# Kernel optimization log

Measured on AMD Instinct MI355X. Metric: run time of the kernel, lower is better.

The kernel has to match this reference:

```python
import jax, jax.numpy as jnp
import numpy as np

B, S, D_IN, D_OUT, H = 4, 2048, 1024, 1024, 16
HD = D_OUT // H


def setup_inputs() -> dict:
    key = jax.random.key(0)
    ks = jax.random.split(key, 6)
    sc_in = 1.0 / np.sqrt(D_IN)
    sc_out = 1.0 / np.sqrt(D_OUT)
    return {
        "x": jax.random.normal(ks[0], (B, S, D_IN), dtype=jnp.float32),
        "Wq": jax.random.normal(ks[1], (D_IN, D_OUT), dtype=jnp.float32) * sc_in,
        "Wk": jax.random.normal(ks[2], (D_IN, D_OUT), dtype=jnp.float32) * sc_in,
        "Wv": jax.random.normal(ks[3], (D_IN, D_OUT), dtype=jnp.float32) * sc_in,
        "Wp": jax.random.normal(ks[4], (D_OUT, D_OUT), dtype=jnp.float32) * sc_out,
        "bp": jax.random.normal(ks[5], (D_OUT,), dtype=jnp.float32) * 0.01,
    }


def reference(x, Wq, Wk, Wv, Wp, bp):
    b, s, _ = x.shape
    # project and split heads: [b, h, s, hd]
    q = (x @ Wq).reshape(b, s, H, HD).transpose(0, 2, 1, 3)
    k = (x @ Wk).reshape(b, s, H, HD).transpose(0, 2, 1, 3)
    v = (x @ Wv).reshape(b, s, H, HD).transpose(0, 2, 1, 3)
    # materialized [b, h, s, s] scores (faithful to the naive module)
    score = jnp.einsum("bhqd,bhkd->bhqk", q, k)
    causal = jnp.tril(jnp.ones((s, s), dtype=bool))
    score = jnp.where(causal, score, -jnp.inf)
    attn = jax.nn.softmax(score / np.sqrt(HD), axis=-1)
    ctx = jnp.einsum("bhqk,bhkd->bhqd", attn, v)
    ctx = ctx.transpose(0, 2, 1, 3).reshape(b, s, D_OUT)
    return ctx @ Wp + bp
```

## Files before the change

kernel.cpp:

```cpp
#include <hip/hip_runtime.h>
#include <hip/hip_bf16.h>
#include <stdint.h>

#define BB   4
#define SS   2048
#define DIN  1024
#define DOUT 1024
#define NH   16
#define HD   64
#define MROWS (BB * SS)

typedef __bf16 bf16x8 __attribute__((ext_vector_type(8)));
typedef float  f32x4  __attribute__((ext_vector_type(4)));

__device__ __forceinline__ unsigned short f2bf(float f) {
  union { float f; uint32_t u; } v; v.f = f;
  uint32_t u = v.u;
  uint32_t r = (u + 0x7fffu + ((u >> 16) & 1u)) >> 16;
  return (unsigned short)r;
}

__device__ __forceinline__ unsigned int cvt_pk_bf16(float lo, float hi) {
  unsigned int r;
  asm("v_cvt_pk_bf16_f32 %0, %1, %2" : "=v"(r) : "v"(lo), "v"(hi));
  return r;
}

#define GLOAD_LDS16(gsrc, ldst)                                                   \
  __builtin_amdgcn_global_load_lds(                                               \
      (const __attribute__((address_space(1))) void*)(gsrc),                      \
      (__attribute__((address_space(3))) void*)(ldst), 16, 0, 0)


__global__ void cvt_x_kernel(const float* __restrict__ in,
                             unsigned short* __restrict__ out, int n4) {
  int i = blockIdx.x * blockDim.x + threadIdx.x;
  int stride = gridDim.x * blockDim.x;
  for (; i < n4; i += stride) {
    float4 f = ((const float4*)in)[i];
    ushort4 o;
    o.x = f2bf(f.x); o.y = f2bf(f.y); o.z = f2bf(f.z); o.w = f2bf(f.w);
    ((ushort4*)out)[i] = o;
  }
}

__global__ void cvt_w_t_kernel(const float* __restrict__ w0,
                               const float* __restrict__ w1,
                               const float* __restrict__ w2,
                               const float* __restrict__ w3,
                               unsigned short* __restrict__ out) {
  __shared__ float tile[32][33];
  const float* src = (blockIdx.z == 0) ? w0 : (blockIdx.z == 1) ? w1
                   : (blockIdx.z == 2) ? w2 : w3;
  unsigned short* dst = out + (size_t)blockIdx.z * (DIN * DOUT);
  int kb = blockIdx.x * 32, nb = blockIdx.y * 32;
  tile[threadIdx.y][threadIdx.x] = src[(size_t)(kb + threadIdx.y) * DOUT + nb + threadIdx.x];
  __syncthreads();
  dst[(size_t)(nb + threadIdx.y) * DIN + kb + threadIdx.x] = f2bf(tile[threadIdx.x][threadIdx.y]);
}

__device__ __forceinline__ void gemm128_core(const unsigned short* __restrict__ A,
                                             const unsigned short* __restrict__ BT,
                                             f32x4 (&acc)[4][4]) {
  extern __shared__ __align__(16) unsigned short sm[];
  const int tid = threadIdx.x, lane = tid & 63, w = tid >> 6;
  const int wm = (w >> 1) * 64, wn = (w & 1) * 64;
  const int g = lane >> 4, c = lane & 15;

#pragma unroll
  for (int mi = 0; mi < 4; mi++)
#pragma unroll
    for (int ni = 0; ni < 4; ni++)
      acc[mi][ni] = (f32x4){0.f, 0.f, 0.f, 0.f};

  const int srow = tid >> 3;
  const int gchunk = (tid & 7) ^ (srow & 7);
  const unsigned short* Ag = A + (size_t)srow * 1024 + gchunk * 8;
  const unsigned short* Bg = BT + (size_t)srow * 1024 + gchunk * 8;
  const int dst8 = tid * 8;

#define STAGE128(kt, buf) do {                                              \
    const int _k = (kt) * 64;                                               \
    _Pragma("unroll") for (int _j = 0; _j < 4; ++_j) {                      \
      GLOAD_LDS16(Ag + (size_t)_j * 32 * 1024 + _k,                         \
                  &sm[(buf) * 8192 + _j * 2048 + dst8]);                    \
      GLOAD_LDS16(Bg + (size_t)_j * 32 * 1024 + _k,                         \
                  &sm[16384 + (buf) * 8192 + _j * 2048 + dst8]);            \
    } } while (0)

  int aoff[4][2], boff[4][2];
#pragma unroll
  for (int mi = 0; mi < 4; mi++)
#pragma unroll
    for (int k2 = 0; k2 < 2; k2++)
      aoff[mi][k2] = (wm + mi * 16 + c) * 64 + (((k2 * 4 + g) ^ (c & 7)) * 8);
#pragma unroll
  for (int ni = 0; ni < 4; ni++)
#pragma unroll
    for (int k2 = 0; k2 < 2; k2++)
      boff[ni][k2] = (wn + ni * 16 + c) * 64 + (((k2 * 4 + g) ^ (c & 7)) * 8);

  STAGE128(0, 0);
  __syncthreads();

#pragma unroll 1
  for (int t = 0; t < 16; ++t) {
    const int buf = t & 1;
    if (t + 1 < 16) STAGE128(t + 1, buf ^ 1);
    const unsigned short* As_ = sm + buf * 8192;
    const unsigned short* Bs_ = sm + 16384 + buf * 8192;
#pragma unroll
    for (int k2 = 0; k2 < 2; k2++) {
      bf16x8 a[4], b[4];
#pragma unroll
      for (int mi = 0; mi < 4; mi++) a[mi] = *(const bf16x8*)&As_[aoff[mi][k2]];
#pragma unroll
      for (int ni = 0; ni < 4; ni++) b[ni] = *(const bf16x8*)&Bs_[boff[ni][k2]];
#pragma unroll
      for (int mi = 0; mi < 4; mi++)
#pragma unroll
        for (int ni = 0; ni < 4; ni++)
          acc[mi][ni] = __builtin_amdgcn_mfma_f32_16x16x32_bf16(a[mi], b[ni], acc[mi][ni], 0, 0, 0);
    }
    __syncthreads();
  }
#undef STAGE128
}

__global__ __launch_bounds__(256, 2) void gemm_qkv_kernel(
    const unsigned short* __restrict__ xb, const unsigned short* __restrict__ wt,
    unsigned short* __restrict__ qs, unsigned short* __restrict__ kbuf,
    unsigned short* __restrict__ vt) {
  const int nT = blockIdx.x, mT = blockIdx.y, z = blockIdx.z;
  f32x4 acc[4][4];
  gemm128_core(xb + (size_t)mT * 128 * 1024,
               wt + (size_t)z * (DIN * DOUT) + (size_t)nT * 128 * 1024, acc);

  const int tid = threadIdx.x, lane = tid & 63, w = tid >> 6;
  const int wm = (w >> 1) * 64, wn = (w & 1) * 64;
  const int g = lane >> 4, c = lane & 15;
  const float scale = (z == 0) ? 0.18033688011112042f : 1.0f;

  if (z < 2) {
    unsigned short* dstQK = (z == 0) ? qs : kbuf;
#pragma unroll
    for (int mi = 0; mi < 4; mi++)
#pragma unroll
      for (int ni = 0; ni < 4; ni++) {
        int n = nT * 128 + wn + ni * 16 + c;
        int h = n >> 6, hd = n & 63;
#pragma unroll
        for (int jj = 0; jj < 4; jj++) {
          int m = mT * 128 + wm + mi * 16 + g * 4 + jj;
          int b = m >> 11, ss = m & 2047;
          dstQK[(((size_t)(b * NH + h)) * SS + ss) * HD + hd] = f2bf(acc[mi][ni][jj] * scale);
        }
      }
  } else {
#pragma unroll
    for (int mi = 0; mi < 4; mi++) {
      int m0 = mT * 128 + wm + mi * 16 + g * 4;
      int b = m0 >> 11, s0 = m0 & 2047;
#pragma unroll
      for (int ni = 0; ni < 4; ni++) {
        int n = nT * 128 + wn + ni * 16 + c;
        int h = n >> 6, hd = n & 63;
        uint2 st;
        st.x = cvt_pk_bf16(acc[mi][ni][0], acc[mi][ni][1]);
        st.y = cvt_pk_bf16(acc[mi][ni][2], acc[mi][ni][3]);
        *(uint2*)&vt[(((size_t)(b * NH + h)) * HD + hd) * SS + s0] = st;
      }
    }
  }
}

__global__ __launch_bounds__(256, 2) void gemm_out_kernel(
    const unsigned short* __restrict__ ctx, const unsigned short* __restrict__ wtp,
    const float* __restrict__ bp, float* __restrict__ out) {
  const int nT = blockIdx.x, mT = blockIdx.y;
  f32x4 acc[4][4];
  gemm128_core(ctx + (size_t)mT * 128 * 1024, wtp + (size_t)nT * 128 * 1024, acc);

  const int tid = threadIdx.x, lane = tid & 63, w = tid >> 6;
  const int wm = (w >> 1) * 64, wn = (w & 1) * 64;
  const int g = lane >> 4, c = lane & 15;
#pragma unroll
  for (int mi = 0; mi < 4; mi++)
#pragma unroll
    for (int ni = 0; ni < 4; ni++) {
      int n = nT * 128 + wn + ni * 16 + c;
      float bias = bp[n];
#pragma unroll
      for (int jj = 0; jj < 4; jj++) {
        int m = mT * 128 + wm + mi * 16 + g * 4 + jj;
        out[(size_t)m * DOUT + n] = acc[mi][ni][jj] + bias;
      }
    }
}

__global__ __launch_bounds__(512) void attn_kernel(
    const unsigned short* __restrict__ qs, const unsigned short* __restrict__ kbuf,
    const unsigned short* __restrict__ vt, unsigned short* __restrict__ ctx) {
  const int pairIdx = blockIdx.x, h = blockIdx.y, b = blockIdx.z;
  const int tid = threadIdx.x, lane = tid & 63, w = tid >> 6;
  const int g = lane >> 4, c = lane & 15;
  const size_t bh = (size_t)(b * NH + h);
  const unsigned short* Q = qs + bh * SS * HD;
  const unsigned short* K = kbuf + bh * SS * HD;
  const unsigned short* V = vt + bh * HD * SS;

  __shared__ __align__(16) unsigned short Klds[2][64 * 64];
  __shared__ __align__(16) unsigned short Vlds[2][64 * 64];

  const int srow = tid >> 3, scol = tid & 7;
  const int sK_w = ((srow & 3) << 1) | ((srow >> 4) & 1);
  const int sV_w = ((srow & 3) << 1) | ((srow >> 2) & 1);
  const int kdst = srow * 64 + ((scol ^ sK_w) * 8);
  const int vdst = srow * 64 + ((scol ^ sV_w) * 8);
  const unsigned short* Kg0 = K + (size_t)srow * HD + scol * 8;
  const unsigned short* Vg0 = V + (size_t)srow * SS + scol * 8;

  int kaoff[4][2], vaoff[4][2];
#pragma unroll
  for (int ni = 0; ni < 4; ni++) {
    int r = (c >> 2) * 16 + ni * 4 + (c & 3);
    int s = ((r & 3) << 1) | ((r >> 4) & 1);
#pragma unroll
    for (int kk = 0; kk < 2; kk++)
      kaoff[ni][kk] = r * 64 + (((kk * 4 + g) ^ s) * 8);
  }
#pragma unroll
  for (int nh = 0; nh < 4; nh++) {
    int r = nh * 16 + c;
    int s = ((r & 3) << 1) | ((r >> 2) & 1);
#pragma unroll
    for (int k2 = 0; k2 < 2; k2++)
      vaoff[nh][k2] = r * 64 + (((2 * g + k2) ^ s) * 8);
  }

#pragma unroll 1
  for (int seg = 0; seg < 2; ++seg) {
    const int qtB = (seg == 0) ? (3 - pairIdx + 4) : pairIdx;
    const int q0 = qtB * 256 + w * 32;
    const int nt = 4 * qtB + 4;
    const int ntw = q0 / 64 + 1;

    bf16x8 aq[2][2];
#pragma unroll
    for (int qf = 0; qf < 2; qf++)
#pragma unroll
      for (int kk = 0; kk < 2; kk++)
        aq[qf][kk] = *(const bf16x8*)&Q[(size_t)(q0 + qf * 16 + c) * HD + kk * 32 + g * 8];

    float m_run[2] = {-3.0e38f, -3.0e38f};
    float l_run[2] = {0.f, 0.f};
    f32x4 acc[2][4];
#pragma unroll
    for (int qf = 0; qf < 2; qf++)
#pragma unroll
      for (int nh = 0; nh < 4; nh++) acc[qf][nh] = (f32x4){0.f, 0.f, 0.f, 0.f};

    {
      uint4 k0 = *(const uint4*)Kg0;
      uint4 v0 = *(const uint4*)Vg0;
      __syncthreads();
      *(uint4*)&Klds[0][kdst] = k0;
      *(uint4*)&Vlds[0][vdst] = v0;
      __syncthreads();
    }
    int cur = 0;

#pragma unroll 1
    for (int t = 0; t < nt; ++t) {
      const bool more = (t + 1 < nt);
      uint4 knx, vnx;
      if (more) {
        knx = *(const uint4*)(Kg0 + (size_t)(t + 1) * 64 * HD);
        vnx = *(const uint4*)(Vg0 + (size_t)(t + 1) * 64);
      }
      if (t < ntw) {
        const unsigned short* Kl = Klds[cur];
        const unsigned short* Vl = Vlds[cur];
        bf16x8 ka[4][2], va[4][2];
#pragma unroll
        for (int ni = 0; ni < 4; ni++)
#pragma unroll
          for (int kk = 0; kk < 2; kk++)
            ka[ni][kk] = *(const bf16x8*)&Kl[kaoff[ni][kk]];
#pragma unroll
        for (int nh = 0; nh < 4; nh++)
#pragma unroll
          for (int k2 = 0; k2 < 2; k2++)
            va[nh][k2] = *(const bf16x8*)&Vl[vaoff[nh][k2]];

        f32x4 sv[2][4];
        __builtin_amdgcn_s_setprio(1);
#pragma unroll
        for (int qf = 0; qf < 2; qf++)
#pragma unroll
          for (int ni = 0; ni < 4; ni++) {
            f32x4 z = (f32x4){0.f, 0.f, 0.f, 0.f};
            z = __builtin_amdgcn_mfma_f32_16x16x32_bf16(ka[ni][0], aq[qf][0], z, 0, 0, 0);
            sv[qf][ni] = __builtin_amdgcn_mfma_f32_16x16x32_bf16(ka[ni][1], aq[qf][1], z, 0, 0, 0);
          }
        __builtin_amdgcn_s_setprio(0);

        if (t == ntw - 1) {
#pragma unroll
          for (int qf = 0; qf < 2; qf++) {
            int q = q0 + qf * 16 + c;
#pragma unroll
            for (int ni = 0; ni < 4; ni++)
#pragma unroll
              for (int jj = 0; jj < 4; jj++) {
                int kvv = t * 64 + g * 16 + ni * 4 + jj;
                if (kvv > q) sv[qf][ni][jj] = -3.0e38f;
              }
          }
        }

#pragma unroll
        for (int qf = 0; qf < 2; qf++) {
          float mx = sv[qf][0][0];
#pragma unroll
          for (int ni = 0; ni < 4; ni++)
#pragma unroll
            for (int jj = 0; jj < 4; jj++) mx = fmaxf(mx, sv[qf][ni][jj]);
          mx = fmaxf(mx, __shfl_xor(mx, 16));
          mx = fmaxf(mx, __shfl_xor(mx, 32));
          float mnew = fmaxf(m_run[qf], mx);
          float al = exp2f(m_run[qf] - mnew);
          m_run[qf] = mnew;
          float rs = 0.f;
#pragma unroll
          for (int ni = 0; ni < 4; ni++)
#pragma unroll
            for (int jj = 0; jj < 4; jj++) {
              float p = exp2f(sv[qf][ni][jj] - mnew);
              sv[qf][ni][jj] = p;
              rs += p;
            }
          rs += __shfl_xor(rs, 16);
          rs += __shfl_xor(rs, 32);
          l_run[qf] = l_run[qf] * al + rs;
#pragma unroll
          for (int nh = 0; nh < 4; nh++) acc[qf][nh] *= al;

          union { unsigned int u[4]; bf16x8 v; } pb0, pb1;
          pb0.u[0] = cvt_pk_bf16(sv[qf][0][0], sv[qf][0][1]);
          pb0.u[1] = cvt_pk_bf16(sv[qf][0][2], sv[qf][0][3]);
          pb0.u[2] = cvt_pk_bf16(sv[qf][1][0], sv[qf][1][1]);
          pb0.u[3] = cvt_pk_bf16(sv[qf][1][2], sv[qf][1][3]);
          pb1.u[0] = cvt_pk_bf16(sv[qf][2][0], sv[qf][2][1]);
          pb1.u[1] = cvt_pk_bf16(sv[qf][2][2], sv[qf][2][3]);
          pb1.u[2] = cvt_pk_bf16(sv[qf][3][0], sv[qf][3][1]);
          pb1.u[3] = cvt_pk_bf16(sv[qf][3][2], sv[qf][3][3]);

          __builtin_amdgcn_s_setprio(1);
#pragma unroll
          for (int nh = 0; nh < 4; nh++) {
            acc[qf][nh] = __builtin_amdgcn_mfma_f32_16x16x32_bf16(va[nh][0], pb0.v, acc[qf][nh], 0, 0, 0);
            acc[qf][nh] = __builtin_amdgcn_mfma_f32_16x16x32_bf16(va[nh][1], pb1.v, acc[qf][nh], 0, 0, 0);
          }
          __builtin_amdgcn_s_setprio(0);
        }
      }
      if (more) {
        *(uint4*)&Klds[cur ^ 1][kdst] = knx;
        *(uint4*)&Vlds[cur ^ 1][vdst] = vnx;
        __syncthreads();
        cur ^= 1;
      }
    }

#pragma unroll
    for (int qf = 0; qf < 2; qf++) {
      float inv = 1.0f / l_run[qf];
      size_t rowoff = ((size_t)b * SS + q0 + qf * 16 + c) * DOUT + h * HD;
#pragma unroll
      for (int nh = 0; nh < 4; nh++) {
        uint2 st;
        st.x = cvt_pk_bf16(acc[qf][nh][0] * inv, acc[qf][nh][1] * inv);
        st.y = cvt_pk_bf16(acc[qf][nh][2] * inv, acc[qf][nh][3] * inv);
        *(uint2*)&ctx[rowoff + nh * 16 + g * 4] = st;
      }
    }
  }
}


extern "C" void kernel_launch(void* const* d_in, const int* in_sizes, int n_in,
                              void* d_out, int out_size, void* d_ws, size_t ws_size,
                              hipStream_t stream) {
  const float* x  = (const float*)d_in[0];
  const float* Wq = (const float*)d_in[1];
  const float* Wk = (const float*)d_in[2];
  const float* Wv = (const float*)d_in[3];
  const float* Wp = (const float*)d_in[4];
  const float* bp = (const float*)d_in[5];
  float* out = (float*)d_out;

  unsigned short* ws = (unsigned short*)d_ws;
  unsigned short* xb = ws;
  unsigned short* wt = xb + (size_t)MROWS * DIN;
  unsigned short* qs = wt + (size_t)4 * DIN * DOUT;
  unsigned short* kb = qs + (size_t)MROWS * DOUT;
  unsigned short* vt = kb + (size_t)MROWS * DOUT;
  unsigned short* ctx = xb;

  const int kLds = 64 * 1024;
  (void)hipFuncSetAttribute((const void*)gemm_qkv_kernel,
                            hipFuncAttributeMaxDynamicSharedMemorySize, kLds);
  (void)hipFuncSetAttribute((const void*)gemm_out_kernel,
                            hipFuncAttributeMaxDynamicSharedMemorySize, kLds);

  cvt_x_kernel<<<4096, 256, 0, stream>>>(x, xb, (MROWS * DIN) / 4);
  cvt_w_t_kernel<<<dim3(32, 32, 4), dim3(32, 32), 0, stream>>>(Wq, Wk, Wv, Wp, wt);
  gemm_qkv_kernel<<<dim3(8, 64, 3), 256, kLds, stream>>>(xb, wt, qs, kb, vt);
  attn_kernel<<<dim3(4, NH, BB), 512, 0, stream>>>(qs, kb, vt, ctx);
  gemm_out_kernel<<<dim3(8, 64), 256, kLds, stream>>>(ctx, wt + (size_t)3 * DIN * DOUT, bp, out);
}
```

Measured before the change: 194.6 us.

## Split attention blocks into 256-thread halves and add lazy softmax rescaling

```diff
diff --git a/kernel.cpp b/kernel.cpp
--- a/kernel.cpp
+++ b/kernel.cpp
@@ -198,10 +198,11 @@
     }
 }
 
-__global__ __launch_bounds__(512) void attn_kernel(
+__global__ __launch_bounds__(256) void attn_kernel(
     const unsigned short* __restrict__ qs, const unsigned short* __restrict__ kbuf,
     const unsigned short* __restrict__ vt, unsigned short* __restrict__ ctx) {
-  const int pairIdx = blockIdx.x, h = blockIdx.y, b = blockIdx.z;
+  const int pairIdx = blockIdx.x >> 1, sub = blockIdx.x & 1;
+  const int h = blockIdx.y, b = blockIdx.z;
   const int tid = threadIdx.x, lane = tid & 63, w = tid >> 6;
   const int g = lane >> 4, c = lane & 15;
   const size_t bh = (size_t)(b * NH + h);
@@ -212,13 +213,15 @@
   __shared__ __align__(16) unsigned short Klds[2][64 * 64];
   __shared__ __align__(16) unsigned short Vlds[2][64 * 64];
 
-  const int srow = tid >> 3, scol = tid & 7;
+  const int srow = tid >> 2, ch0 = (tid & 3) * 2;
   const int sK_w = ((srow & 3) << 1) | ((srow >> 4) & 1);
   const int sV_w = ((srow & 3) << 1) | ((srow >> 2) & 1);
-  const int kdst = srow * 64 + ((scol ^ sK_w) * 8);
-  const int vdst = srow * 64 + ((scol ^ sV_w) * 8);
-  const unsigned short* Kg0 = K + (size_t)srow * HD + scol * 8;
-  const unsigned short* Vg0 = V + (size_t)srow * SS + scol * 8;
+  const int kd0 = srow * 64 + ((ch0 ^ sK_w) * 8);
+  const int kd1 = srow * 64 + (((ch0 + 1) ^ sK_w) * 8);
+  const int vd0 = srow * 64 + ((ch0 ^ sV_w) * 8);
+  const int vd1 = srow * 64 + (((ch0 + 1) ^ sV_w) * 8);
+  const unsigned short* Kg0 = K + (size_t)srow * HD + ch0 * 8;
+  const unsigned short* Vg0 = V + (size_t)srow * SS + ch0 * 8;
 
   int kaoff[4][2], vaoff[4][2];
 #pragma unroll
@@ -240,9 +243,9 @@
 
 #pragma unroll 1
   for (int seg = 0; seg < 2; ++seg) {
-    const int qtB = (seg == 0) ? (3 - pairIdx + 4) : pairIdx;
-    const int q0 = qtB * 256 + w * 32;
-    const int nt = 4 * qtB + 4;
+    const int qtB = (seg == 0) ? (7 - pairIdx) : pairIdx;
+    const int q0 = qtB * 256 + sub * 128 + w * 32;
+    const int nt = 4 * qtB + 2 * sub + 2;
     const int ntw = q0 / 64 + 1;
 
     bf16x8 aq[2][2];
@@ -261,11 +264,15 @@
       for (int nh = 0; nh < 4; nh++) acc[qf][nh] = (f32x4){0.f, 0.f, 0.f, 0.f};
 
     {
-      uint4 k0 = *(const uint4*)Kg0;
-      uint4 v0 = *(const uint4*)Vg0;
+      uint4 ka_ = *(const uint4*)Kg0;
+      uint4 kb_ = *(const uint4*)(Kg0 + 8);
+      uint4 va_ = *(const uint4*)Vg0;
+      uint4 vb_ = *(const uint4*)(Vg0 + 8);
       __syncthreads();
-      *(uint4*)&Klds[0][kdst] = k0;
-      *(uint4*)&Vlds[0][vdst] = v0;
+      *(uint4*)&Klds[0][kd0] = ka_;
+      *(uint4*)&Klds[0][kd1] = kb_;
+      *(uint4*)&Vlds[0][vd0] = va_;
+      *(uint4*)&Vlds[0][vd1] = vb_;
       __syncthreads();
     }
     int cur = 0;
@@ -273,10 +280,12 @@
 #pragma unroll 1
     for (int t = 0; t < nt; ++t) {
       const bool more = (t + 1 < nt);
-      uint4 knx, vnx;
+      uint4 knx0, knx1, vnx0, vnx1;
       if (more) {
-        knx = *(const uint4*)(Kg0 + (size_t)(t + 1) * 64 * HD);
-        vnx = *(const uint4*)(Vg0 + (size_t)(t + 1) * 64);
+        knx0 = *(const uint4*)(Kg0 + (size_t)(t + 1) * 64 * HD);
+        knx1 = *(const uint4*)(Kg0 + (size_t)(t + 1) * 64 * HD + 8);
+        vnx0 = *(const uint4*)(Vg0 + (t + 1) * 64);
+        vnx1 = *(const uint4*)(Vg0 + (t + 1) * 64 + 8);
       }
       if (t < ntw) {
         const unsigned short* Kl = Klds[cur];
@@ -321,30 +330,37 @@
 
 #pragma unroll
         for (int qf = 0; qf < 2; qf++) {
-          float mx = sv[qf][0][0];
-#pragma unroll
-          for (int ni = 0; ni < 4; ni++)
-#pragma unroll
-            for (int jj = 0; jj < 4; jj++) mx = fmaxf(mx, sv[qf][ni][jj]);
+          float mx = fmaxf(fmaxf(sv[qf][0][0], sv[qf][0][1]), sv[qf][0][2]);
+          mx = fmaxf(fmaxf(mx, sv[qf][0][3]), sv[qf][1][0]);
+          mx = fmaxf(fmaxf(mx, sv[qf][1][1]), sv[qf][1][2]);
+          mx = fmaxf(fmaxf(mx, sv[qf][1][3]), sv[qf][2][0]);
+          mx = fmaxf(fmaxf(mx, sv[qf][2][1]), sv[qf][2][2]);
+          mx = fmaxf(fmaxf(mx, sv[qf][2][3]), sv[qf][3][0]);
+          mx = fmaxf(fmaxf(mx, sv[qf][3][1]), sv[qf][3][2]);
+          mx = fmaxf(mx, sv[qf][3][3]);
           mx = fmaxf(mx, __shfl_xor(mx, 16));
           mx = fmaxf(mx, __shfl_xor(mx, 32));
-          float mnew = fmaxf(m_run[qf], mx);
-          float al = exp2f(m_run[qf] - mnew);
-          m_run[qf] = mnew;
+          if (__any(mx > m_run[qf] + 8.0f)) {
+            float mnew = fmaxf(m_run[qf], mx);
+            float al = exp2f(m_run[qf] - mnew);
+            m_run[qf] = mnew;
+            l_run[qf] *= al;
+#pragma unroll
+            for (int nh = 0; nh < 4; nh++) acc[qf][nh] *= al;
+          }
+          const float m0 = m_run[qf];
           float rs = 0.f;
 #pragma unroll
           for (int ni = 0; ni < 4; ni++)
 #pragma unroll
             for (int jj = 0; jj < 4; jj++) {
-              float p = exp2f(sv[qf][ni][jj] - mnew);
+              float p = exp2f(sv[qf][ni][jj] - m0);
               sv[qf][ni][jj] = p;
               rs += p;
             }
           rs += __shfl_xor(rs, 16);
           rs += __shfl_xor(rs, 32);
-          l_run[qf] = l_run[qf] * al + rs;
-#pragma unroll
-          for (int nh = 0; nh < 4; nh++) acc[qf][nh] *= al;
+          l_run[qf] += rs;
 
           union { unsigned int u[4]; bf16x8 v; } pb0, pb1;
           pb0.u[0] = cvt_pk_bf16(sv[qf][0][0], sv[qf][0][1]);
@@ -366,8 +382,10 @@
         }
       }
       if (more) {
-        *(uint4*)&Klds[cur ^ 1][kdst] = knx;
-        *(uint4*)&Vlds[cur ^ 1][vdst] = vnx;
+        *(uint4*)&Klds[cur ^ 1][kd0] = knx0;
+        *(uint4*)&Klds[cur ^ 1][kd1] = knx1;
+        *(uint4*)&Vlds[cur ^ 1][vd0] = vnx0;
+        *(uint4*)&Vlds[cur ^ 1][vd1] = vnx1;
         __syncthreads();
         cur ^= 1;
       }
@@ -417,6 +435,6 @@
   cvt_x_kernel<<<4096, 256, 0, stream>>>(x, xb, (MROWS * DIN) / 4);
   cvt_w_t_kernel<<<dim3(32, 32, 4), dim3(32, 32), 0, stream>>>(Wq, Wk, Wv, Wp, wt);
   gemm_qkv_kernel<<<dim3(8, 64, 3), 256, kLds, stream>>>(xb, wt, qs, kb, vt);
-  attn_kernel<<<dim3(4, NH, BB), 512, 0, stream>>>(qs, kb, vt, ctx);
+  attn_kernel<<<dim3(8, NH, BB), 256, 0, stream>>>(qs, kb, vt, ctx);
   gemm_out_kernel<<<dim3(8, 64), 256, kLds, stream>>>(ctx, wt + (size_t)3 * DIN * DOUT, bp, out);
 }
```

Result: slower. 251.1 us (+29.1%).
